# Optimization experiments

Measured on AMD Instinct MI355X. Metric: run time of the kernel, lower is better.

## Reference

```python
import jax, jax.numpy as jnp
import numpy as np

EPS = 1e-5

def inorm(x):
    # instance norm over time (last) axis; torch.std is unbiased (ddof=1)
    m = jnp.mean(x, axis=-1, keepdims=True)
    s = jnp.sqrt(jnp.var(x, axis=-1, ddof=1, keepdims=True))
    return (x - m) / (s + EPS)

def tinorm(x):
    # time-wise instance norm: normalize over channel axis (dim=1)
    m = jnp.mean(x, axis=1, keepdims=True)
    s = jnp.sqrt(jnp.var(x, axis=1, ddof=1, keepdims=True))
    return (x - m) / (s + EPS)

def adaptive_norm(src, trg, wq, wk, wv, norm_fn):
    # src, trg: [B,C,T]; wq/wk/wv: [out,in] as in nn.Linear
    temp = src.shape[1] ** 0.5
    q = jnp.einsum('bct,oc->bto', norm_fn(src), wq)        # [B,Ts,C]
    k = jnp.einsum('bct,oc->bto', norm_fn(trg), wk)        # [B,Tt,C]
    v = jnp.einsum('bct,oc->bto', trg, wv)                 # [B,Tt,C]
    attn = jax.nn.softmax(jnp.einsum('bsc,btc->bst', q / temp, k), axis=-1)
    mean = jnp.einsum('bst,btc->bsc', attn, v)             # attn-weighted mean
    var = jax.nn.relu(jnp.einsum('bst,btc->bsc', attn, v * v) - mean * mean)
    mean_c = jnp.mean(mean, axis=1)[:, :, None]            # [B,C,1]
    std_c = jnp.sqrt(jnp.mean(var, axis=1))[:, :, None]    # [B,C,1]
    return std_c * inorm(src) + mean_c

def sap(x, w, b):
    # self-attention pooling over axis 1; x: [B,N,C], w: [C], b: [1]
    a = jax.nn.softmax(jnp.einsum('bnc,c->bn', x, w) + b, axis=-1)
    return jnp.einsum('bnc,bn->bc', x, a)

def setup_inputs():
    key = jax.random.key(0)
    ks = jax.random.split(key, 24)
    B, C, Ts, Tt, S = 4, 512, 2048, 2048, 2048
    sc = 1.0 / np.sqrt(C).astype(np.float32)
    return {
        'src': jax.random.normal(ks[0], (B, C, Ts), jnp.float32),
        'trg': jax.random.normal(ks[1], (B, C, Tt), jnp.float32),
        'means': jax.random.normal(ks[2], (B, S, C), jnp.float32),
        'stds': jax.random.uniform(ks[3], (B, S, C), jnp.float32),
        'wq_t': jax.random.normal(ks[4], (C, C), jnp.float32) * sc,
        'wk_t': jax.random.normal(ks[5], (C, C), jnp.float32) * sc,
        'wv_t': jax.random.normal(ks[6], (C, C), jnp.float32) * sc,
        'wq_c': jax.random.normal(ks[7], (C, C), jnp.float32) * sc,
        'wk_c': jax.random.normal(ks[8], (C, C), jnp.float32) * sc,
        'wv_c': jax.random.normal(ks[9], (C, C), jnp.float32) * sc,
        'conv1_w': jax.random.normal(ks[10], (C, 2 * C), jnp.float32) * sc,
        'conv1_b': jax.random.normal(ks[11], (C,), jnp.float32) * 0.02,
        'conv2_w': jax.random.normal(ks[12], (C, C, 3), jnp.float32) * sc,
        'bn_g': jax.random.uniform(ks[13], (C,), jnp.float32, 0.5, 1.5),
        'bn_b': jax.random.normal(ks[14], (C,), jnp.float32) * 0.05,
        'bn_m': jax.random.normal(ks[15], (C,), jnp.float32) * 0.1,
        'bn_v': jax.random.uniform(ks[16], (C,), jnp.float32, 0.5, 1.5),
        'msap_w': jax.random.normal(ks[17], (C,), jnp.float32) * sc,
        'msap_b': jax.random.normal(ks[18], (1,), jnp.float32) * 0.02,
        'ssap_w': jax.random.normal(ks[19], (C,), jnp.float32) * sc,
        'ssap_b': jax.random.normal(ks[20], (1,), jnp.float32) * 0.02,
    }

def reference(src, trg, means, stds, wq_t, wk_t, wv_t, wq_c, wk_c, wv_c,
              conv1_w, conv1_b, conv2_w, bn_g, bn_b, bn_m, bn_v,
              msap_w, msap_b, ssap_w, ssap_b):
    src1 = adaptive_norm(src, trg, wq_t, wk_t, wv_t, tinorm)   # TAN
    src2 = adaptive_norm(src, trg, wq_c, wk_c, wv_c, inorm)    # CAN
    x = jnp.concatenate([src1, src2], axis=1)                  # [B,2C,T]
    # conv1: kernel_size=1 -> pointwise GEMM
    x = jnp.einsum('bct,oc->bot', x, conv1_w) + conv1_b[None, :, None]
    # conv2: Conv1d(k=3, pad=1, bias=False) + BatchNorm1d(eval) + ReLU
    x = jax.lax.conv_general_dilated(x, conv2_w, (1,), 'SAME',
                                     dimension_numbers=('NCH', 'OIH', 'NCH'))
    x = (x - bn_m[None, :, None]) * jax.lax.rsqrt(bn_v[None, :, None] + EPS)
    x = x * bn_g[None, :, None] + bn_b[None, :, None]
    x = jax.nn.relu(x)
    # GLAN
    mean = sap(means, msap_w, msap_b)[:, :, None]              # [B,C,1]
    std = sap(stds, ssap_w, ssap_b)[:, :, None]                # [B,C,1]
    return inorm(x) * std + mean
```

## Files before the change

### kernel.cpp

```cpp
#include <hip/hip_runtime.h>
#include <cstdint>
#include <cstddef>

#define B_ 4
#define C_ 512
#define T_ 2048
#define S_ 2048
#define EPSF 1e-5f

typedef __bf16 bf16;
typedef __attribute__((ext_vector_type(8))) __bf16 bf16x8;
typedef __attribute__((ext_vector_type(4))) float f32x4;

__device__ __forceinline__ bf16 f2b(float f){ return (bf16)f; }
__device__ __forceinline__ float b2f(bf16 h){ return (float)h; }

__device__ __forceinline__ void gl_lds16(const void* g, void* l){
  __builtin_amdgcn_global_load_lds((__attribute__((address_space(1))) void*)(g),
                                   (__attribute__((address_space(3))) void*)(l), 16, 0, 0);
}

__device__ __forceinline__ float wave_sum(float v){
#pragma unroll
  for (int o = 32; o; o >>= 1) v += __shfl_xor(v, o, 64);
  return v;
}
__device__ __forceinline__ float wave_max(float v){
#pragma unroll
  for (int o = 32; o; o >>= 1) v = fmaxf(v, __shfl_xor(v, o, 64));
  return v;
}

template<int EPI, int TNW>
__global__ void __launch_bounds__(256) gemm_nt(
    const bf16* __restrict__ A, const bf16* __restrict__ Bm, void* __restrict__ Cout,
    int K, int lda, int ldb, int ldc,
    long long sA, long long sB, long long sC, long long sCb,
    int zdivA, int zmodB, float scale,
    const float* __restrict__ rs, const float* __restrict__ rsh,
    const float* __restrict__ cbias,
    float* __restrict__ osum, float* __restrict__ osum2, long long sRs)
{
  constexpr int TN = TNW*32;
  __shared__ alignas(16) bf16 lA[128*64];
  __shared__ alignas(16) bf16 lB[TN*64];
  const int tid = threadIdx.x;
  const int z = blockIdx.z;
  const bf16* Ab = A + (long long)(z / zdivA) * sA;
  const bf16* Bb = Bm + (long long)(z % zmodB) * sB;
  const int m0 = blockIdx.y*128, n0 = blockIdx.x*TN;
  const int lane = tid & 63, wvi = tid >> 6;
  const int wm = wvi >> 1, wn = wvi & 1;

  f32x4 acc[4][TNW] = {};

  const int lrow = tid >> 3;
  const int lcol = ((tid ^ lrow) & 7) * 8;
  const bf16* pa = Ab + (long long)(m0 + lrow)*lda + lcol;
  const bf16* pb = Bb + (long long)(n0 + lrow)*ldb + lcol;
  char* sa = (char*)lA + tid*16;
  char* sb = (char*)lB + tid*16;

  for (int k0 = 0; k0 < K; k0 += 64) {
#pragma unroll
    for (int it = 0; it < 4; ++it)
      gl_lds16(pa + (long long)it*32*lda + k0, sa + it*4096);
#pragma unroll
    for (int it = 0; it < TNW; ++it)
      gl_lds16(pb + (long long)it*32*ldb + k0, sb + it*4096);
    __syncthreads();
#pragma unroll
    for (int ks = 0; ks < 2; ++ks) {
      const int kq = ks*4 + (lane >> 4);
      bf16x8 af[4], bfr[TNW];
#pragma unroll
      for (int mt = 0; mt < 4; ++mt) {
        int r = wm*64 + mt*16 + (lane & 15);
        af[mt] = *(const bf16x8*)&lA[r*64 + ((kq ^ (r & 7))*8)];
      }
#pragma unroll
      for (int nt = 0; nt < TNW; ++nt) {
        int r = wn*(TNW*16) + nt*16 + (lane & 15);
        bfr[nt] = *(const bf16x8*)&lB[r*64 + ((kq ^ (r & 7))*8)];
      }
#pragma unroll
      for (int mt = 0; mt < 4; ++mt)
#pragma unroll
        for (int nt = 0; nt < TNW; ++nt)
          acc[mt][nt] = __builtin_amdgcn_mfma_f32_16x16x32_bf16(af[mt], bfr[nt], acc[mt][nt], 0, 0, 0);
    }
    __syncthreads();
  }

  if (EPI == 3) {
    float* red1 = (float*)lA;
    float* red2 = red1 + 4*TNW*16;
    const int cr = (lane >> 4)*4;
    float linv[4][4];
#pragma unroll
    for (int mt = 0; mt < 4; ++mt)
#pragma unroll
      for (int i = 0; i < 4; ++i)
        linv[mt][i] = 1.f / rs[(long long)z*sRs + (m0 + wm*64 + mt*16 + cr + i)];
    float s1[TNW], s2[TNW];
#pragma unroll
    for (int nt = 0; nt < TNW; ++nt) {
      s1[nt] = 0.f; s2[nt] = 0.f;
#pragma unroll
      for (int mt = 0; mt < 4; ++mt)
#pragma unroll
        for (int i = 0; i < 4; ++i) {
          float v = acc[mt][nt][i] * linv[mt][i];
          s1[nt] += v; s2[nt] += v*v;
        }
      s1[nt] += __shfl_xor(s1[nt], 16, 64);
      s1[nt] += __shfl_xor(s1[nt], 32, 64);
      s2[nt] += __shfl_xor(s2[nt], 16, 64);
      s2[nt] += __shfl_xor(s2[nt], 32, 64);
    }
    if (lane < 16) {
#pragma unroll
      for (int nt = 0; nt < TNW; ++nt) {
        red1[(wvi*TNW + nt)*16 + lane] = s1[nt];
        red2[(wvi*TNW + nt)*16 + lane] = s2[nt];
      }
    }
    __syncthreads();
    if (tid < 2*TN) {
      const int which = tid >= TN;
      const int col = tid - which*TN;
      const int wn2 = col / (TNW*16), rem = col % (TNW*16);
      const float* rr = which ? red2 : red1;
      float v = rr[wn2*(TNW*16) + rem] + rr[(2+wn2)*(TNW*16) + rem];
      float* dst = which ? osum2 : osum;
      atomicAdd(&dst[sCb*z + n0 + col], v);
    }
    return;
  }

  const int cr = (lane >> 4)*4, cc = lane & 15;
#pragma unroll
  for (int mt = 0; mt < 4; ++mt) {
#pragma unroll
    for (int i = 0; i < 4; ++i) {
      const int mm = m0 + wm*64 + mt*16 + cr + i;
      float rsum = 0.f, rsum2 = 0.f;
#pragma unroll
      for (int nt = 0; nt < TNW; ++nt) {
        const int nn = n0 + wn*(TNW*16) + nt*16 + cc;
        float v = acc[mt][nt][i];
        const long long co = sC*z + (long long)mm*ldc + nn;
        if (EPI == 0) {
          v *= scale;
          if (cbias) v += cbias[sCb*z + nn];
          ((bf16*)Cout)[co] = f2b(v);
        } else if (EPI == 2) {
          v = fmaxf(v*rs[mm] + rsh[mm], 0.f);
          ((float*)Cout)[co] = v;
          rsum += v; rsum2 += v*v;
        } else if (EPI == 4) {
          v = __expf(v);
          ((bf16*)Cout)[co] = f2b(v);
          rsum += v;
        }
      }
      if (EPI == 2 || EPI == 4) {
        rsum += __shfl_xor(rsum, 1, 64); rsum += __shfl_xor(rsum, 2, 64);
        rsum += __shfl_xor(rsum, 4, 64); rsum += __shfl_xor(rsum, 8, 64);
        if (EPI == 2) {
          rsum2 += __shfl_xor(rsum2, 1, 64); rsum2 += __shfl_xor(rsum2, 2, 64);
          rsum2 += __shfl_xor(rsum2, 4, 64); rsum2 += __shfl_xor(rsum2, 8, 64);
        }
        if (cc == 0) {
          atomicAdd(&osum[(long long)z*sRs + mm], rsum);
          if (EPI == 2) atomicAdd(&osum2[(long long)z*sRs + mm], rsum2);
        }
      }
    }
  }
}

__global__ void __launch_bounds__(256) row_stats_k(const float* __restrict__ X1,
    const float* __restrict__ X2, float* __restrict__ Mo, float* __restrict__ So, int n1)
{
  __shared__ float r1[4], r2[4];
  const int row = blockIdx.x;
  const float* x = (row < n1) ? X1 + (long long)row*T_ : X2 + (long long)(row-n1)*T_;
  float s1 = 0.f, s2 = 0.f;
  for (int i = threadIdx.x; i < T_; i += 256){ float v = x[i]; s1 += v; s2 += v*v; }
  s1 = wave_sum(s1); s2 = wave_sum(s2);
  const int lane = threadIdx.x & 63, w = threadIdx.x >> 6;
  if (!lane){ r1[w] = s1; r2[w] = s2; }
  __syncthreads();
  if (threadIdx.x == 0){
    s1 = r1[0]+r1[1]+r1[2]+r1[3];
    s2 = r2[0]+r2[1]+r2[2]+r2[3];
    float m = s1 * (1.f/T_);
    float var = (s2 - s1*m) * (1.f/(T_-1));
    Mo[row] = m; So[row] = sqrtf(fmaxf(var, 0.f));
  }
}

__global__ void __launch_bounds__(256) col_stats_k(const float* __restrict__ src,
    const float* __restrict__ trg, float* __restrict__ Mo, float* __restrict__ So)
{
  __shared__ float r1[4][64], r2[4][64];
  const int z = blockIdx.y, t0 = blockIdx.x*64;
  const float* X = (z < B_) ? src : trg;
  const int b = z & (B_-1);
  const int tl = threadIdx.x & 63, cg = threadIdx.x >> 6;
  float s1 = 0.f, s2 = 0.f;
  for (int c = cg; c < C_; c += 4) {
    float v = X[((long long)b*C_ + c)*T_ + t0 + tl];
    s1 += v; s2 += v*v;
  }
  r1[cg][tl] = s1; r2[cg][tl] = s2;
  __syncthreads();
  if (cg == 0) {
    s1 = r1[0][tl]+r1[1][tl]+r1[2][tl]+r1[3][tl];
    s2 = r2[0][tl]+r2[1][tl]+r2[2][tl]+r2[3][tl];
    float m = s1 * (1.f/C_);
    float var = (s2 - s1*m) * (1.f/(C_-1));
    Mo[z*T_ + t0 + tl] = m;
    So[z*T_ + t0 + tl] = sqrtf(fmaxf(var, 0.f));
  }
}

__global__ void __launch_bounds__(256) transform_k(const float* __restrict__ src,
    const float* __restrict__ trg,
    const float* __restrict__ tnm, const float* __restrict__ tns,
    const float* __restrict__ inm, const float* __restrict__ ins,
    bf16* __restrict__ NSt, bf16* __restrict__ NSc,
    bf16* __restrict__ NTt, bf16* __restrict__ NTc, bf16* __restrict__ TTr)
{
  __shared__ float tile[32][33];
  const int z = blockIdx.z, t0 = blockIdx.x*32, c0 = blockIdx.y*32;
  const int is_t = z >= B_, b = z & (B_-1);
  const float* X = is_t ? trg : src;
  const int tx = threadIdx.x, ty = threadIdx.y;
#pragma unroll
  for (int r = 0; r < 4; ++r) {
    int ci = ty + r*8;
    tile[ci][tx] = X[((long long)b*C_ + c0 + ci)*T_ + t0 + tx];
  }
  __syncthreads();
#pragma unroll
  for (int r = 0; r < 4; ++r) {
    int tj = ty + r*8, ci = tx;
    float v = tile[ci][tj];
    int gt = t0 + tj, gc = c0 + ci;
    float a = (v - tnm[z*T_ + gt]) / (tns[z*T_ + gt] + EPSF);
    float d = (v - inm[z*C_ + gc]) / (ins[z*C_ + gc] + EPSF);
    long long o = ((long long)b*T_ + gt)*C_ + gc;
    if (is_t) { NTt[o] = f2b(a); NTc[o] = f2b(d); TTr[o] = f2b(v); }
    else      { NSt[o] = f2b(a); NSc[o] = f2b(d); }
  }
}

__global__ void __launch_bounds__(256) softmax_row_k(const float* __restrict__ X, float* __restrict__ O)
{
  __shared__ float red[4];
  const long long row = blockIdx.x;
  const float* x = X + row*T_ + threadIdx.x*8;
  float v[8];
  f32x4 a0 = *(const f32x4*)x;
  f32x4 a1 = *(const f32x4*)(x + 4);
#pragma unroll
  for (int j = 0; j < 4; ++j){ v[j] = a0[j]; v[4+j] = a1[j]; }
  float m = -3.4e38f;
#pragma unroll
  for (int j = 0; j < 8; ++j) m = fmaxf(m, v[j]);
  m = wave_max(m);
  const int lane = threadIdx.x & 63, w = threadIdx.x >> 6;
  if (!lane) red[w] = m;
  __syncthreads();
  m = fmaxf(fmaxf(red[0], red[1]), fmaxf(red[2], red[3]));
  __syncthreads();
  float s = 0.f;
#pragma unroll
  for (int j = 0; j < 8; ++j){ v[j] = __expf(v[j] - m); s += v[j]; }
  s = wave_sum(s);
  if (!lane) red[w] = s;
  __syncthreads();
  s = red[0]+red[1]+red[2]+red[3];
  const float inv = 1.f/s;
  float* o = O + row*T_ + threadIdx.x*8;
#pragma unroll
  for (int j = 0; j < 8; ++j) o[j] = v[j]*inv;
}

__global__ void __launch_bounds__(256) colsum_k(const bf16* __restrict__ P,
    const float* __restrict__ l, float* __restrict__ cs)
{
  __shared__ float linv[256];
  const int t = blockIdx.x*256 + threadIdx.x;
  const int z = blockIdx.z;
  const long long s0 = (long long)blockIdx.y*256;
  linv[threadIdx.x] = 1.f / l[(long long)z*S_ + s0 + threadIdx.x];
  __syncthreads();
  const bf16* p = P + ((long long)z*S_ + s0)*T_ + t;
  float a = 0.f;
  for (int s = 0; s < 256; ++s) a += b2f(p[(long long)s*T_]) * linv[s];
  atomicAdd(&cs[z*T_ + t], a);
}

__global__ void __launch_bounds__(256) vv_fin_k(const float* __restrict__ cs,
    const bf16* __restrict__ VT, const float* __restrict__ msum,
    const float* __restrict__ m2sum, float* __restrict__ meanc, float* __restrict__ stdc)
{
  __shared__ float r1[4];
  const int c = blockIdx.x, z = blockIdx.y;
  const bf16* vr = VT + ((long long)z*C_ + c)*T_;
  const float* w = cs + z*T_;
  float a = 0.f;
  for (int t = threadIdx.x; t < T_; t += 256){ float v = b2f(vr[t]); a += w[t]*v*v; }
  a = wave_sum(a);
  const int lane = threadIdx.x & 63, wq = threadIdx.x >> 6;
  if (!lane) r1[wq] = a;
  __syncthreads();
  if (threadIdx.x == 0){
    a = r1[0]+r1[1]+r1[2]+r1[3];
    const int idx = z*C_ + c;
    meanc[idx] = msum[idx] * (1.f/S_);
    float var = (a - m2sum[idx]) * (1.f/S_);
    stdc[idx] = sqrtf(fmaxf(var, 0.f));
  }
}

__global__ void __launch_bounds__(256) weff_k(const float* __restrict__ w1,
    const float* __restrict__ b1, const float* __restrict__ sdt, const float* __restrict__ sdc,
    const float* __restrict__ mct, const float* __restrict__ mcc,
    bf16* __restrict__ Weff, float* __restrict__ beff)
{
  __shared__ float r1[4];
  const int o = blockIdx.x, b = blockIdx.y;
  float accb = 0.f;
  for (int c = threadIdx.x; c < C_; c += 256) {
    float wa = w1[o*2*C_ + c], wb = w1[o*2*C_ + C_ + c];
    Weff[((long long)(b*C_ + o))*C_ + c] = f2b(wa*sdt[b*C_+c] + wb*sdc[b*C_+c]);
    accb += wa*mct[b*C_+c] + wb*mcc[b*C_+c];
  }
  accb = wave_sum(accb);
  const int lane = threadIdx.x & 63, w = threadIdx.x >> 6;
  if (!lane) r1[w] = accb;
  __syncthreads();
  if (threadIdx.x == 0) beff[b*C_ + o] = b1[o] + r1[0]+r1[1]+r1[2]+r1[3];
}

__global__ void __launch_bounds__(256) w2r_k(const float* __restrict__ w2,
    const float* __restrict__ g, const float* __restrict__ be,
    const float* __restrict__ mu, const float* __restrict__ va,
    bf16* __restrict__ W2r, float* __restrict__ bnsc, float* __restrict__ bnsh)
{
  const int o = blockIdx.x;
  for (int c = threadIdx.x; c < C_; c += 256)
#pragma unroll
    for (int dt = 0; dt < 3; ++dt)
      W2r[(long long)o*3*C_ + dt*C_ + c] = f2b(w2[((long long)o*C_ + c)*3 + dt]);
  if (threadIdx.x == 0) {
    float s = g[o] * rsqrtf(va[o] + EPSF);
    bnsc[o] = s;
    bnsh[o] = be[o] - mu[o]*s;
  }
}

__global__ void __launch_bounds__(256) cast6_k(const float* __restrict__ a0,
    const float* __restrict__ a1, const float* __restrict__ a2, const float* __restrict__ a3,
    const float* __restrict__ a4, const float* __restrict__ a5, bf16* __restrict__ o)
{
  const int i = blockIdx.x*256 + threadIdx.x;
  const int slot = i >> 18;
  const float* srcs[6] = {a0,a1,a2,a3,a4,a5};
  const float sc = (slot < 2) ? 0.044194173824159216f : 1.f;
  o[i] = f2b(srcs[slot][i & 262143] * sc);
}

__global__ void __launch_bounds__(256) zero_pad_k(bf16* __restrict__ x1p)
{
  const int i = blockIdx.x*256 + threadIdx.x;
  const int b = i >> 10, rem = i & 1023;
  const long long row = (rem >> 9) ? (T_+1) : 0;
  const int c = rem & (C_-1);
  x1p[((long long)b*(T_+2) + row)*C_ + c] = f2b(0.f);
}

__global__ void __launch_bounds__(256) zero_f32_k(float* __restrict__ p)
{
  p[blockIdx.x*256 + threadIdx.x] = 0.f;
}

__global__ void __launch_bounds__(256) sap_logit_k(const float* __restrict__ means,
    const float* __restrict__ stds, const float* __restrict__ mw, const float* __restrict__ sw,
    const float* __restrict__ mb, const float* __restrict__ sb, float* __restrict__ out)
{
  const int n = blockIdx.x*4 + (threadIdx.x >> 6);
  const int z = blockIdx.y;
  const int sel = z >= B_, b = z & (B_-1);
  const float* x = sel ? stds : means;
  const float* w = sel ? sw : mw;
  const int lane = threadIdx.x & 63;
  const float* p = x + ((long long)b*S_ + n)*C_;
  float a = 0.f;
  for (int c = lane; c < C_; c += 64) a += p[c]*w[c];
  a = wave_sum(a);
  if (!lane) out[z*S_ + n] = a + (sel ? sb[0] : mb[0]);
}

__global__ void __launch_bounds__(256) sap_wsum_k(const float* __restrict__ means,
    const float* __restrict__ stds, const float* __restrict__ a, float* __restrict__ out)
{
  const int c = blockIdx.x*256 + threadIdx.x;
  const int z = blockIdx.z;
  const int sel = z >= B_, b = z & (B_-1);
  const float* x = sel ? stds : means;
  const long long n0 = (long long)blockIdx.y*256;
  const float* p = x + ((long long)b*S_ + n0)*C_ + c;
  const float* aw = a + z*S_ + n0;
  float acc = 0.f;
  for (int n = 0; n < 256; ++n) acc += p[(long long)n*C_] * aw[n];
  atomicAdd(&out[z*C_ + c], acc);
}

__global__ void __launch_bounds__(256) final_k(const float* __restrict__ y,
    const float* __restrict__ ysum, const float* __restrict__ y2sum,
    const float* __restrict__ sapms, float* __restrict__ out)
{
  const long long i = (long long)(blockIdx.x*256 + threadIdx.x) * 4;
  const long long r = i >> 11;
  const float s1 = ysum[r], s2 = y2sum[r];
  const float m = s1 * (1.f/T_);
  const float var = (s2 - s1*m) * (1.f/(T_-1));
  const float inv = 1.f/(sqrtf(fmaxf(var, 0.f)) + EPSF);
  const float mn = sapms[r], sd = sapms[B_*C_ + r];
  const f32x4 v = *(const f32x4*)(y + i);
  f32x4 o;
#pragma unroll
  for (int j = 0; j < 4; ++j) o[j] = (v[j] - m)*inv*sd + mn;
  *(f32x4*)(out + i) = o;
}

extern "C" void kernel_launch(void* const* d_in, const int* in_sizes, int n_in,
                              void* d_out, int out_size, void* d_ws, size_t ws_size,
                              hipStream_t stream)
{
  (void)in_sizes; (void)n_in; (void)out_size; (void)ws_size;
  const float* src    = (const float*)d_in[0];
  const float* trg    = (const float*)d_in[1];
  const float* means  = (const float*)d_in[2];
  const float* stds   = (const float*)d_in[3];
  const float* conv1w = (const float*)d_in[10];
  const float* conv1b = (const float*)d_in[11];
  const float* conv2w = (const float*)d_in[12];
  const float* bn_g   = (const float*)d_in[13];
  const float* bn_b   = (const float*)d_in[14];
  const float* bn_m   = (const float*)d_in[15];
  const float* bn_v   = (const float*)d_in[16];
  const float* msap_w = (const float*)d_in[17];
  const float* msap_b = (const float*)d_in[18];
  const float* ssap_w = (const float*)d_in[19];
  const float* ssap_b = (const float*)d_in[20];

  const long long BTC = (long long)B_*T_*C_;

  char* p = (char*)d_ws;
  auto take = [&](size_t n)->char*{ char* r = p; p += (n + 255) & ~(size_t)255; return r; };

  bf16* NSc = (bf16*)take(BTC*2);
  bf16* P2  = (bf16*)take((size_t)2*B_*S_*T_*2);
  bf16* NSt = P2;
  bf16* NTc = P2 + BTC;
  bf16* NTt = P2 + 2*BTC;
  bf16* TTr = P2 + 3*BTC;
  bf16* QK4 = (bf16*)take((size_t)4*BTC*2);
  bf16* VT2 = (bf16*)take((size_t)2*BTC*2);
  bf16* WQb = (bf16*)take((size_t)6*C_*C_*2);
  bf16* Weff= (bf16*)take((size_t)B_*C_*C_*2);
  bf16* W2r = (bf16*)take((size_t)C_*3*C_*2);
  bf16* x1p = (bf16*)take((size_t)B_*(T_+2)*C_*2);
  float* y  = (float*)take((size_t)B_*C_*T_*4);
  float* colsum = (float*)take(2*B_*T_*4);
  float* msum   = (float*)take(2*B_*C_*4);
  float* m2sum  = (float*)take(2*B_*C_*4);
  float* sapms  = (float*)take(2*B_*C_*4);
  float* lrow   = (float*)take(2*B_*S_*4);
  float* ysum   = (float*)take(B_*C_*4);
  float* y2sum  = (float*)take(B_*C_*4);
  float* tnm = (float*)take(2*B_*T_*4);
  float* tns = (float*)take(2*B_*T_*4);
  float* inm = (float*)take(2*B_*C_*4);
  float* ins = (float*)take(2*B_*C_*4);
  float* meanc = (float*)take(2*B_*C_*4);
  float* stdc  = (float*)take(2*B_*C_*4);
  float* beff  = (float*)take(B_*C_*4);
  float* bnsc  = (float*)take(C_*4);
  float* bnsh  = (float*)take(C_*4);
  float* sapl  = (float*)take(2*B_*S_*4);
  float* sapa  = (float*)take(2*B_*S_*4);

  dim3 blk(256);

  cast6_k<<<6144, blk, 0, stream>>>((const float*)d_in[7], (const float*)d_in[4],
      (const float*)d_in[8], (const float*)d_in[5], (const float*)d_in[9],
      (const float*)d_in[6], WQb);
  w2r_k<<<C_, blk, 0, stream>>>(conv2w, bn_g, bn_b, bn_m, bn_v, W2r, bnsc, bnsh);
  row_stats_k<<<2*B_*C_, blk, 0, stream>>>(src, trg, inm, ins, B_*C_);
  col_stats_k<<<dim3(T_/64, 2*B_), blk, 0, stream>>>(src, trg, tnm, tns);
  transform_k<<<dim3(T_/32, C_/32, 2*B_), dim3(32,8), 0, stream>>>(src, trg,
      tnm, tns, inm, ins, NSt, NSc, NTt, NTc, TTr);
  zero_pad_k<<<16, blk, 0, stream>>>(x1p);
  zero_f32_k<<<192, blk, 0, stream>>>(colsum);

  gemm_nt<0,4><<<dim3(C_/128, (B_*T_)/128, 4), blk, 0, stream>>>(NSc, WQb, QK4,
      C_, C_, C_, C_, BTC, (long long)C_*C_, BTC, 0, 1, 8, 1.f,
      nullptr, nullptr, nullptr, nullptr, nullptr, 0);
  gemm_nt<0,2><<<dim3(T_/64, C_/128, 8), blk, 0, stream>>>(WQb + (size_t)4*C_*C_, TTr, VT2,
      C_, C_, C_, T_, (long long)C_*C_, (long long)T_*C_, (long long)C_*T_, 0, 4, 4, 1.f,
      nullptr, nullptr, nullptr, nullptr, nullptr, 0);
  gemm_nt<4,4><<<dim3(T_/128, T_/128, 8), blk, 0, stream>>>(QK4, QK4 + 2*BTC, P2,
      C_, C_, C_, T_, (long long)T_*C_, (long long)T_*C_, (long long)S_*T_, 0, 1, 8, 1.f,
      nullptr, nullptr, nullptr, lrow, nullptr, S_);
  colsum_k<<<dim3(T_/256, S_/256, 8), blk, 0, stream>>>(P2, lrow, colsum);
  gemm_nt<3,4><<<dim3(C_/128, S_/128, 8), blk, 0, stream>>>(P2, VT2, nullptr,
      T_, T_, T_, 0, (long long)S_*T_, (long long)C_*T_, 0, C_, 1, 8, 1.f,
      lrow, nullptr, nullptr, msum, m2sum, S_);
  vv_fin_k<<<dim3(C_, 2*B_), blk, 0, stream>>>(colsum, VT2, msum, m2sum, meanc, stdc);

  weff_k<<<dim3(C_, B_), blk, 0, stream>>>(conv1w, conv1b,
      stdc + B_*C_, stdc, meanc + B_*C_, meanc, Weff, beff);
  gemm_nt<0,2><<<dim3(C_/64, T_/128, B_), blk, 0, stream>>>(NSc, Weff, x1p + C_,
      C_, C_, C_, C_, (long long)T_*C_, (long long)C_*C_, (long long)(T_+2)*C_, C_,
      1, 8, 1.f, nullptr, nullptr, beff, nullptr, nullptr, 0);
  gemm_nt<2,2><<<dim3(T_/64, C_/128, B_), blk, 0, stream>>>(W2r, x1p, y,
      3*C_, 3*C_, C_, T_, 0, (long long)(T_+2)*C_, (long long)C_*T_, 0,
      1, 8, 1.f, bnsc, bnsh, nullptr, ysum, y2sum, C_);

  sap_logit_k<<<dim3(S_/4, 2*B_), blk, 0, stream>>>(means, stds, msap_w, ssap_w,
      msap_b, ssap_b, sapl);
  softmax_row_k<<<2*B_, blk, 0, stream>>>(sapl, sapa);
  sap_wsum_k<<<dim3(C_/256, S_/256, 2*B_), blk, 0, stream>>>(means, stds, sapa, sapms);

  final_k<<<4096, blk, 0, stream>>>(y, ysum, y2sum, sapms, (float*)d_out);
}
```

Baseline: 477.4 us.

## Add dedicated 256x256-tile QK^T exp kernel with double-buffered LDS staging

Replaces the generic gemm_nt<4,4> launch for the Q·K^T score GEMM with a specialized kernel. It uses 512 threads, 256x256 output tiles, and a 64-wide K slice double-buffered in 128KB of LDS via global_load_lds. Reads are XOR-swizzled and MFMA issue is raised with s_setprio. The larger tile raises arithmetic intensity and cuts global traffic for the largest GEMM. The exp epilogue and row-sum atomics are kept. In exchange it uses a lot of LDS and registers, which limits occupancy, and it writes P with strided scattered bf16 stores.

New measurement: 470.3 us. About the same (-1.5%).

```diff
diff --git a/kernel.cpp b/kernel.cpp
--- a/kernel.cpp
+++ b/kernel.cpp
@@ -176,6 +176,101 @@
           if (EPI == 2) atomicAdd(&osum2[(long long)z*sRs + mm], rsum2);
         }
       }
+    }
+  }
+}
+
+__global__ void __launch_bounds__(512, 2) qk_exp_k(
+    const bf16* __restrict__ Q, const bf16* __restrict__ Km,
+    bf16* __restrict__ P, float* __restrict__ lsum)
+{
+  __shared__ alignas(16) char lds[131072];
+  const int tid = threadIdx.x;
+  const int z = blockIdx.z;
+  const int m0 = blockIdx.y * 256, n0 = blockIdx.x * 256;
+  const int lane = tid & 63, wvi = tid >> 6;
+  const int wm = wvi >> 2, wn = wvi & 3;
+  const int l15 = lane & 15, lq = lane >> 4;
+  const int swz = l15 & 7;
+
+  f32x4 acc[8][4] = {};
+
+  const int lr = tid >> 3;
+  const int lc = ((tid ^ lr) & 7) * 8;
+  const bf16* pa = Q  + (long long)z*(2048LL*512) + (long long)(m0 + lr)*512 + lc;
+  const bf16* pb = Km + (long long)z*(2048LL*512) + (long long)(n0 + lr)*512 + lc;
+
+  auto STAGE = [&](int b, int kt) {
+    char* da = (char*)lds + b*65536 + tid*16;
+    const bf16* ga = pa + kt*64;
+    const bf16* gb = pb + kt*64;
+#pragma unroll
+    for (int it = 0; it < 4; ++it) gl_lds16(ga + it*64*512, da + it*8192);
+#pragma unroll
+    for (int it = 0; it < 4; ++it) gl_lds16(gb + it*64*512, da + 32768 + it*8192);
+  };
+
+  STAGE(0, 0);
+  for (int kt = 0; kt < 8; ++kt) {
+    const int cur = kt & 1;
+    if (kt < 7) {
+      STAGE(cur ^ 1, kt + 1);
+      asm volatile("s_waitcnt vmcnt(8)" ::: "memory");
+    } else {
+      asm volatile("s_waitcnt vmcnt(0)" ::: "memory");
+    }
+    __builtin_amdgcn_s_barrier();
+
+    const bf16* lA = (const bf16*)(lds + cur*65536);
+    const bf16* lB = lA + 16384;
+
+    bf16x8 af[4], bfr[4];
+#pragma unroll
+    for (int half = 0; half < 4; ++half) {
+      const int ks = half >> 1, mg = (half & 1) * 4;
+      const int kq = ks*4 + lq;
+      const int ko = (kq ^ swz) * 8;
+      if ((half & 1) == 0) {
+#pragma unroll
+        for (int nt = 0; nt < 4; ++nt)
+          bfr[nt] = *(const bf16x8*)&lB[(wn*64 + nt*16 + l15)*64 + ko];
+      }
+#pragma unroll
+      for (int mt = 0; mt < 4; ++mt)
+        af[mt] = *(const bf16x8*)&lA[(wm*128 + (mg + mt)*16 + l15)*64 + ko];
+      __builtin_amdgcn_s_barrier();
+      __builtin_amdgcn_s_setprio(1);
+#pragma unroll
+      for (int mt = 0; mt < 4; ++mt)
+#pragma unroll
+        for (int nt = 0; nt < 4; ++nt)
+          acc[mg + mt][nt] = __builtin_amdgcn_mfma_f32_16x16x32_bf16(
+              af[mt], bfr[nt], acc[mg + mt][nt], 0, 0, 0);
+      __builtin_amdgcn_s_setprio(0);
+      __builtin_amdgcn_s_barrier();
+    }
+  }
+
+  const long long zT = (long long)z * 2048;
+  bf16* Cb = P + zT * 2048;
+  float* lrw = lsum + zT;
+  const int cr = lq * 4;
+#pragma unroll
+  for (int mt = 0; mt < 8; ++mt) {
+#pragma unroll
+    for (int i = 0; i < 4; ++i) {
+      const int mm = m0 + wm*128 + mt*16 + cr + i;
+      float rsum = 0.f;
+#pragma unroll
+      for (int nt = 0; nt < 4; ++nt) {
+        const int nn = n0 + wn*64 + nt*16 + l15;
+        float v = __expf(acc[mt][nt][i]);
+        Cb[(long long)mm*2048 + nn] = f2b(v);
+        rsum += v;
+      }
+      rsum += __shfl_xor(rsum, 1, 64); rsum += __shfl_xor(rsum, 2, 64);
+      rsum += __shfl_xor(rsum, 4, 64); rsum += __shfl_xor(rsum, 8, 64);
+      if (l15 == 0) atomicAdd(&lrw[mm], rsum);
     }
   }
 }
@@ -516,9 +611,8 @@
   gemm_nt<0,2><<<dim3(T_/64, C_/128, 8), blk, 0, stream>>>(WQb + (size_t)4*C_*C_, TTr, VT2,
       C_, C_, C_, T_, (long long)C_*C_, (long long)T_*C_, (long long)C_*T_, 0, 4, 4, 1.f,
       nullptr, nullptr, nullptr, nullptr, nullptr, 0);
-  gemm_nt<4,4><<<dim3(T_/128, T_/128, 8), blk, 0, stream>>>(QK4, QK4 + 2*BTC, P2,
-      C_, C_, C_, T_, (long long)T_*C_, (long long)T_*C_, (long long)S_*T_, 0, 1, 8, 1.f,
-      nullptr, nullptr, nullptr, lrow, nullptr, S_);
+  qk_exp_k<<<dim3(T_/256, T_/256, 8), dim3(512), 0, stream>>>(QK4, QK4 + 2*BTC,
+      P2, lrow);
   colsum_k<<<dim3(T_/256, S_/256, 8), blk, 0, stream>>>(P2, lrow, colsum);
   gemm_nt<3,4><<<dim3(C_/128, S_/128, 8), blk, 0, stream>>>(P2, VT2, nullptr,
       T_, T_, T_, 0, (long long)S_*T_, (long long)C_*T_, 0, C_, 1, 8, 1.f,
```
